# Kernel optimization log

Hardware: AMD Instinct MI355X
Metric: run time of the kernel (lower is better)

## Reference

```python
import jax, jax.numpy as jnp
import numpy as np

N = 524288
NUM_LEVELS = 16
FEATS = 2
LOG2_T = 19
TABLE = 1 << LOG2_T
MIN_RES, MAX_RES = 16, 1024
PRIMES = np.array([1, 2654435761, 805459861], dtype=np.uint32)
_growth = np.exp((np.log(MAX_RES) - np.log(MIN_RES)) / (NUM_LEVELS - 1))
SCALINGS = np.floor(MIN_RES * _growth ** np.arange(NUM_LEVELS)).astype(np.float32)  # [L]


def hash_encode(positions, table):
    # positions [N,3] in [0,1]; table [L*T, F]
    scaled = positions[:, None, :] * jnp.asarray(SCALINGS)[None, :, None]  # [N,L,3]
    fl = jnp.floor(scaled)
    ce = jnp.ceil(scaled)
    offset = scaled - fl  # [N,L,3]
    primes = jnp.asarray(PRIMES)  # [3] uint32
    lvl_off = jnp.arange(NUM_LEVELS, dtype=jnp.uint32) * jnp.uint32(TABLE)  # [L]
    out = jnp.zeros(scaled.shape[:2] + (FEATS,), scaled.dtype)
    for corner in range(8):
        bits = np.array([(corner >> d) & 1 for d in range(3)], dtype=np.float32)
        coord = jnp.where(jnp.asarray(bits, dtype=bool), ce, fl)
        h = coord.astype(jnp.int32).astype(jnp.uint32) * primes  # [N,L,3]
        h = h[..., 0] ^ h[..., 1] ^ h[..., 2]
        idx = ((h & jnp.uint32(TABLE - 1)) + lvl_off).astype(jnp.int32)  # [N,L]
        b = jnp.asarray(bits)
        w = jnp.prod(b * offset + (1.0 - b) * (1.0 - offset), axis=-1, keepdims=True)  # [N,L,1]
        out = out + w * table[idx]
    return out.reshape(out.shape[0], NUM_LEVELS * FEATS)  # [N,32]


def nerf_encode(d):
    # NeRFEncoding: 4 freqs in 2**linspace(0,4,4), include_input=True -> 27 dims
    freqs = 2.0 ** jnp.linspace(0.0, 4.0, 4)
    scaled = (2.0 * jnp.pi * d)[..., None] * freqs  # [N,3,4]
    scaled = scaled.reshape(d.shape[0], -1)  # [N,12]
    enc = jnp.sin(jnp.concatenate([scaled, scaled + jnp.pi / 2.0], axis=-1))  # [N,24]
    return jnp.concatenate([enc, d], axis=-1)  # [N,27]


def setup_inputs() -> dict:
    key = jax.random.key(0)
    ks = jax.random.split(key, 16)
    w = lambda k, i, o: jax.random.normal(k, (i, o), jnp.float32) * (1.0 / np.sqrt(i))
    return {
        "positions": jax.random.uniform(ks[0], (N, 3), jnp.float32),
        "directions": jax.random.normal(ks[1], (N, 3), jnp.float32),
        "hash_table": (jax.random.uniform(ks[2], (NUM_LEVELS * TABLE, FEATS), jnp.float32) * 2.0 - 1.0) * 1e-3,
        "w0": w(ks[3], 32, 64), "b0": jnp.zeros((64,), jnp.float32),
        "w1": w(ks[4], 64, 64), "b1": jnp.zeros((64,), jnp.float32),
        "w2": w(ks[5], 64, 64), "b2": jnp.zeros((64,), jnp.float32),
        "wr": w(ks[6], 91, 32), "br": jnp.zeros((32,), jnp.float32),
        "wc": w(ks[7], 32, 3), "bc": jnp.zeros((3,), jnp.float32),
        "wd": w(ks[8], 64, 1), "bd": jnp.zeros((1,), jnp.float32),
    }


def reference(positions, directions, hash_table, w0, b0, w1, b1, w2, b2, wr, br, wc, bc, wd, bd):
    enc_xyz = hash_encode(positions, hash_table)  # [N,32]
    enc_dir = nerf_encode(directions)  # [N,27]
    h = jax.nn.relu(enc_xyz @ w0 + b0)
    h = jax.nn.relu(h @ w1 + b1)
    base = h @ w2 + b2  # [N,64], linear out (out_activation=None)
    rgb_h = jnp.concatenate([enc_dir, base], axis=-1) @ wr + br  # [N,32], single layer
    rgb = jax.nn.sigmoid(rgb_h @ wc + bc)  # [N,3]
    density = jax.nn.softplus(base @ wd + bd)  # [N,1]
    return jnp.concatenate([rgb, density], axis=-1)  # [N,4]
```

## Files before the change

kernel.cpp:

```cpp
#include <hip/hip_runtime.h>
#include <math.h>

#define NPTS 524288
#define LOG2T 19
#define TSIZE (1u << LOG2T)
#define TMASK (TSIZE - 1u)

typedef unsigned int uint32;
typedef unsigned short ushort16;

typedef __attribute__((ext_vector_type(8))) short short8;
typedef __attribute__((ext_vector_type(4))) float f32x4;

__device__ __forceinline__ float bf2f(ushort16 u) {
    union { uint32 i; float f; } v; v.i = ((uint32)u) << 16; return v.f;
}
__device__ __forceinline__ ushort16 f2bf(float f) {
    union { float f; uint32 i; } v; v.f = f;
    uint32 r = v.i + 0x7fffu + ((v.i >> 16) & 1u);
    return (ushort16)(r >> 16);
}
__device__ __forceinline__ uint32 pack2(float a, float b) {
    return (uint32)f2bf(a) | ((uint32)f2bf(b) << 16);
}
__device__ __forceinline__ float ldin(const void* p, int i, bool f32) {
    return f32 ? ((const float*)p)[i] : bf2f(((const ushort16*)p)[i]);
}

struct Scal16 { float s[16]; };
struct Freq4  { float f[4]; };
struct HashP  { float s[16]; int dD[8]; int doff[8]; };
struct DenseP { int dD[6]; int pfx[7]; };

__global__ __launch_bounds__(256) void k_cvt10(const void* __restrict__ pos,
                                               const float4* __restrict__ tbl,
                                               uint4* __restrict__ tbl2F) {
    __shared__ int sFlag;
    int tid = threadIdx.x;
    if (tid < 64) {
        const ushort16* ph = (const ushort16*)pos;
        float v0 = bf2f(ph[tid]), v1 = bf2f(ph[tid + 64]);
        bool odd = !(fabsf(v0) <= 4.f) || !(fabsf(v1) <= 4.f);
        unsigned long long m = __ballot(odd);
        if (tid == 0) sFlag = (m != 0ull) ? 1 : 0;
    }
    __syncthreads();
    if (sFlag == 0) return;
    size_t g = (size_t)blockIdx.x * 256 + tid;
    float4 v0 = tbl[(size_t)3 * TSIZE + 2 * g];
    float4 v1 = tbl[(size_t)3 * TSIZE + 2 * g + 1];
    uint4 o;
    o.x = pack2(v0.x, v0.y); o.y = pack2(v0.z, v0.w);
    o.z = pack2(v1.x, v1.y); o.w = pack2(v1.z, v1.w);
    tbl2F[g] = o;
}

__global__ __launch_bounds__(256) void k_dense(const void* __restrict__ pos,
                                               const void* __restrict__ tbl,
                                               uint4* __restrict__ dense4,
                                               DenseP dp) {
    __shared__ int sFlag;
    int tid = threadIdx.x;
    if (tid < 64) {
        const ushort16* ph = (const ushort16*)pos;
        float v0 = bf2f(ph[tid]), v1 = bf2f(ph[tid + 64]);
        bool odd = !(fabsf(v0) <= 4.f) || !(fabsf(v1) <= 4.f);
        unsigned long long m = __ballot(odd);
        if (tid == 0) sFlag = (m != 0ull) ? 1 : 0;
    }
    __syncthreads();
    const bool f32 = (sFlag != 0);

    int e = blockIdx.x * 256 + tid;
    if (e >= dp.pfx[6]) return;
    int l = 0;
#pragma unroll
    for (int k = 1; k < 6; ++k) l += (e >= dp.pfx[k]) ? 1 : 0;
    int c = e - dp.pfx[l];
    int D = dp.dD[l], D2 = D * D;
    int cz = c / D2; int rm = c - cz * D2;
    int cy = rm / D; int cx = rm - cy * D;

    uint32 base = (uint32)l << LOG2T;
    uint32 hz  = (uint32)cz * 805459861u;
    uint32 hy0 = (uint32)cy * 2654435761u;
    uint32 hy1 = (uint32)(cy + 1) * 2654435761u;
    uint32 h00 = ((((uint32)cx)       ^ hy0 ^ hz) & TMASK) + base;
    uint32 h10 = ((((uint32)(cx + 1)) ^ hy0 ^ hz) & TMASK) + base;
    uint32 h01 = ((((uint32)cx)       ^ hy1 ^ hz) & TMASK) + base;
    uint32 h11 = ((((uint32)(cx + 1)) ^ hy1 ^ hz) & TMASK) + base;

    uint4 o;
    if (f32) {
        const float2* t2 = (const float2*)tbl;
        float2 a = t2[h00], b = t2[h10], cc = t2[h01], d = t2[h11];
        o.x = pack2(a.x, a.y); o.y = pack2(b.x, b.y);
        o.z = pack2(cc.x, cc.y); o.w = pack2(d.x, d.y);
    } else {
        const uint32* t1 = (const uint32*)tbl;
        o.x = t1[h00]; o.y = t1[h10]; o.z = t1[h01]; o.w = t1[h11];
    }
    dense4[e] = o;
}

__global__ __launch_bounds__(256) void k_denseEnc(const void* __restrict__ pos,
                                                  const uint4* __restrict__ dense4,
                                                  uint32* __restrict__ enc,
                                                  HashP hp) {
    __shared__ __align__(16) uint4 sPosQ[192];
    __shared__ int sFlag;
    int tid = threadIdx.x;
    if (tid < 64) {
        const ushort16* ph = (const ushort16*)pos;
        float v0 = bf2f(ph[tid]), v1 = bf2f(ph[tid + 64]);
        bool odd = !(fabsf(v0) <= 4.f) || !(fabsf(v1) <= 4.f);
        unsigned long long m = __ballot(odd);
        if (tid == 0) sFlag = (m != 0ull) ? 1 : 0;
    }
    __syncthreads();
    const bool f32 = (sFlag != 0);

    int p0 = blockIdx.x * 256;
    int pt = p0 + tid;

    {
        int n16 = f32 ? 192 : 96;
        const uint4* src = (const uint4*)((const char*)pos + (size_t)p0 * (f32 ? 12 : 6));
        for (int i = tid; i < n16; i += 256) sPosQ[i] = src[i];
    }
    __syncthreads();

    float x, y, z;
    if (f32) {
        const float* pf = (const float*)sPosQ;
        x = pf[3 * tid]; y = pf[3 * tid + 1]; z = pf[3 * tid + 2];
    } else {
        const ushort16* ph2 = (const ushort16*)sPosQ;
        x = bf2f(ph2[3 * tid]); y = bf2f(ph2[3 * tid + 1]); z = bf2f(ph2[3 * tid + 2]);
    }

#pragma unroll
    for (int l = 0; l < 6; ++l) {
        float s = hp.s[l];
        float sx = x * s, sy = y * s, sz = z * s;
        float fx = floorf(sx), fy = floorf(sy), fz = floorf(sz);
        float cx = ceilf(sx), cy = ceilf(sy), cz = ceilf(sz);
        float ox = sx - fx, oy = sy - fy, oz = sz - fz;
        float wx0 = 1.f - ox, wy0 = 1.f - oy, wz0 = 1.f - oz;

        int D = hp.dD[l], D2 = D * D;
        int fxi = (int)fx, fyi = (int)fy, fzi = (int)fz;
        bool dxb = ((int)cx != fxi);
        bool dyb = ((int)cy != fyi);
        bool dzb = ((int)cz != fzi);
        const uint4* dp4 = dense4 + hp.doff[l];
        int i0 = fxi + fyi * D + fzi * D2;
        uint4 P0 = dp4[i0];
        uint4 P1 = dp4[i0 + (dzb ? D2 : 0)];

        float a0 = 0.f, a1 = 0.f;
        {
            uint32 fv = P0.x, cv = dxb ? P0.y : P0.x;
            float w = wy0 * wz0;
            a0 += w * (wx0 * bf2f((ushort16)(fv & 0xffffu)) + ox * bf2f((ushort16)(cv & 0xffffu)));
            a1 += w * (wx0 * bf2f((ushort16)(fv >> 16))     + ox * bf2f((ushort16)(cv >> 16)));
        }
        {
            uint32 fv = dyb ? P0.z : P0.x;
            uint32 cv = dyb ? (dxb ? P0.w : P0.z) : (dxb ? P0.y : P0.x);
            float w = oy * wz0;
            a0 += w * (wx0 * bf2f((ushort16)(fv & 0xffffu)) + ox * bf2f((ushort16)(cv & 0xffffu)));
            a1 += w * (wx0 * bf2f((ushort16)(fv >> 16))     + ox * bf2f((ushort16)(cv >> 16)));
        }
        {
            uint32 fv = P1.x, cv = dxb ? P1.y : P1.x;
            float w = wy0 * oz;
            a0 += w * (wx0 * bf2f((ushort16)(fv & 0xffffu)) + ox * bf2f((ushort16)(cv & 0xffffu)));
            a1 += w * (wx0 * bf2f((ushort16)(fv >> 16))     + ox * bf2f((ushort16)(cv >> 16)));
        }
        {
            uint32 fv = dyb ? P1.z : P1.x;
            uint32 cv = dyb ? (dxb ? P1.w : P1.z) : (dxb ? P1.y : P1.x);
            float w = oy * oz;
            a0 += w * (wx0 * bf2f((ushort16)(fv & 0xffffu)) + ox * bf2f((ushort16)(cv & 0xffffu)));
            a1 += w * (wx0 * bf2f((ushort16)(fv >> 16))     + ox * bf2f((ushort16)(cv >> 16)));
        }
        enc[(size_t)l * NPTS + pt] = pack2(a0, a1);
    }
}

__global__ __launch_bounds__(256) void k_hashB(const void* __restrict__ pos,
                                               const void* __restrict__ tbl,
                                               const uint32* __restrict__ tbl2F,
                                               uint32* __restrict__ enc,
                                               HashP hp) {
    __shared__ __align__(16) uint4 sPosQ[192];
    __shared__ int sFlag;
    int tid = threadIdx.x;
    if (tid < 64) {
        const ushort16* ph = (const ushort16*)pos;
        float v0 = bf2f(ph[tid]), v1 = bf2f(ph[tid + 64]);
        bool odd = !(fabsf(v0) <= 4.f) || !(fabsf(v1) <= 4.f);
        unsigned long long m = __ballot(odd);
        if (tid == 0) sFlag = (m != 0ull) ? 1 : 0;
    }
    __syncthreads();
    const bool f32 = (sFlag != 0);

    int xcd = blockIdx.x & 7;
    int slot = blockIdx.x >> 3;
    int W = xcd * 2560 + slot;
    int lvl = 6 + (W >> 11);
    int chunk = W & 2047;
    int p0 = chunk * 256;
    int pt = p0 + tid;

    {
        int n16 = f32 ? 192 : 96;
        const uint4* src = (const uint4*)((const char*)pos + (size_t)p0 * (f32 ? 12 : 6));
        for (int i = tid; i < n16; i += 256) sPosQ[i] = src[i];
    }
    __syncthreads();

    float x, y, z;
    if (f32) {
        const float* pf = (const float*)sPosQ;
        x = pf[3 * tid]; y = pf[3 * tid + 1]; z = pf[3 * tid + 2];
    } else {
        const ushort16* ph2 = (const ushort16*)sPosQ;
        x = bf2f(ph2[3 * tid]); y = bf2f(ph2[3 * tid + 1]); z = bf2f(ph2[3 * tid + 2]);
    }

    float s = hp.s[lvl];
    float sx = x * s, sy = y * s, sz = z * s;
    float fx = floorf(sx), fy = floorf(sy), fz = floorf(sz);
    float cx = ceilf(sx), cy = ceilf(sy), cz = ceilf(sz);
    float ox = sx - fx, oy = sy - fy, oz = sz - fz;
    float wx0 = 1.f - ox, wy0 = 1.f - oy, wz0 = 1.f - oz;

    const uint32* tp; uint32 base;
    if (f32) { tp = tbl2F; base = (uint32)(lvl - 6) << LOG2T; }
    else     { tp = (const uint32*)tbl; base = (uint32)lvl << LOG2T; }
    uint32 hx0 = (uint32)(int)fx;
    uint32 hx1 = (uint32)(int)cx;
    uint32 hy0 = (uint32)(int)fy * 2654435761u;
    uint32 hy1 = (uint32)(int)cy * 2654435761u;
    uint32 hz0 = (uint32)(int)fz * 805459861u;
    uint32 hz1 = (uint32)(int)cz * 805459861u;

    float a0 = 0.f, a1 = 0.f;
#pragma unroll
    for (int yz = 0; yz < 4; ++yz) {
        uint32 m = ((yz & 1) ? hy1 : hy0) ^ ((yz & 2) ? hz1 : hz0);
        float wyz = ((yz & 1) ? oy : wy0) * ((yz & 2) ? oz : wz0);
        uint32 i0 = ((hx0 ^ m) & TMASK) + base;
        uint32 i1 = ((hx1 ^ m) & TMASK) + base;
        uint32 d0, d1;
        if (i1 == (i0 ^ 1u)) {
            uint2 pv = *(const uint2*)(tp + (i0 & ~1u));
            d0 = (i0 & 1u) ? pv.y : pv.x;
            d1 = (i0 & 1u) ? pv.x : pv.y;
        } else {
            d0 = tp[i0]; d1 = tp[i1];
        }
        a0 += wyz * (wx0 * bf2f((ushort16)(d0 & 0xffffu)) + ox * bf2f((ushort16)(d1 & 0xffffu)));
        a1 += wyz * (wx0 * bf2f((ushort16)(d0 >> 16))     + ox * bf2f((ushort16)(d1 >> 16)));
    }
    enc[(size_t)lvl * NPTS + pt] = pack2(a0, a1);
}

__global__ __launch_bounds__(256) void k_hash(const void* __restrict__ pos,
                                              const void* __restrict__ tbl,
                                              uint32* __restrict__ enc,
                                              Scal16 sc) {
    __shared__ int sFlag;
    int tid = threadIdx.x;
    if (tid < 64) {
        const ushort16* ph = (const ushort16*)pos;
        float v0 = bf2f(ph[tid]), v1 = bf2f(ph[tid + 64]);
        bool odd = !(fabsf(v0) <= 4.f) || !(fabsf(v1) <= 4.f);
        unsigned long long m = __ballot(odd);
        if (tid == 0) sFlag = (m != 0ull) ? 1 : 0;
    }
    __syncthreads();
    const bool f32 = (sFlag != 0);

    int lvl = ((blockIdx.x >> 14) << 3) + (blockIdx.x & 7);
    int pt = ((blockIdx.x >> 3) & 2047) * 256 + tid;

    float s = sc.s[lvl];
    float x = ldin(pos, 3 * pt, f32), y = ldin(pos, 3 * pt + 1, f32), z = ldin(pos, 3 * pt + 2, f32);
    float sx = x * s, sy = y * s, sz = z * s;
    float fx = floorf(sx), fy = floorf(sy), fz = floorf(sz);
    float cx = ceilf(sx), cy = ceilf(sy), cz = ceilf(sz);
    float ox = sx - fx, oy = sy - fy, oz = sz - fz;
    uint32 hx0 = (uint32)(int)fx;
    uint32 hx1 = (uint32)(int)cx;
    uint32 hy0 = (uint32)(int)fy * 2654435761u;
    uint32 hy1 = (uint32)(int)cy * 2654435761u;
    uint32 hz0 = (uint32)(int)fz * 805459861u;
    uint32 hz1 = (uint32)(int)cz * 805459861u;
    uint32 base = (uint32)lvl << LOG2T;
    float wx0 = 1.f - ox, wy0 = 1.f - oy, wz0 = 1.f - oz;

    float a0 = 0.f, a1 = 0.f;
    if (f32) {
        const float* tf = (const float*)tbl;
#pragma unroll
        for (int yz = 0; yz < 4; ++yz) {
            uint32 m = ((yz & 1) ? hy1 : hy0) ^ ((yz & 2) ? hz1 : hz0);
            float wyz = ((yz & 1) ? oy : wy0) * ((yz & 2) ? oz : wz0);
            uint32 i0 = ((hx0 ^ m) & TMASK) + base;
            uint32 i1 = ((hx1 ^ m) & TMASK) + base;
            float4 pv = *(const float4*)(tf + (size_t)(i0 & ~1u) * 2);
            bool lo = !(i0 & 1u);
            float f0 = lo ? pv.x : pv.z, f1 = lo ? pv.y : pv.w;
            float c0, c1;
            if (i1 == (i0 ^ 1u)) { c0 = lo ? pv.z : pv.x; c1 = lo ? pv.w : pv.y; }
            else { float2 tv = ((const float2*)tbl)[i1]; c0 = tv.x; c1 = tv.y; }
            a0 += wyz * (wx0 * f0 + ox * c0);
            a1 += wyz * (wx0 * f1 + ox * c1);
        }
    } else {
#pragma unroll
        for (int cr = 0; cr < 8; ++cr) {
            uint32 h = ((cr & 1) ? hx1 : hx0) ^ ((cr & 2) ? hy1 : hy0) ^ ((cr & 4) ? hz1 : hz0);
            uint32 idx = (h & TMASK) + base;
            uint32 dv = ((const uint32*)tbl)[idx];
            float w = ((cr & 1) ? ox : wx0) * ((cr & 2) ? oy : wy0) * ((cr & 4) ? oz : wz0);
            a0 += w * bf2f((ushort16)(dv & 0xffffu));
            a1 += w * bf2f((ushort16)(dv >> 16));
        }
    }
    enc[(size_t)lvl * NPTS + pt] = pack2(a0, a1);
}

#define STRY 72
#define STRW0 40
#define STRW12 72
#define STRWR 104
#define MSTRX 100
#define PPI 128
#define NIT (NPTS / PPI)

__global__ __launch_bounds__(512) void k_mlp(
    const void* __restrict__ pos,
    const uint32* __restrict__ enc, const void* __restrict__ dirs,
    const void* __restrict__ w0, const void* __restrict__ b0,
    const void* __restrict__ w1, const void* __restrict__ b1,
    const void* __restrict__ w2, const void* __restrict__ b2,
    const void* __restrict__ wr, const void* __restrict__ br,
    const void* __restrict__ wc, const void* __restrict__ bc,
    const void* __restrict__ wd, const void* __restrict__ bd,
    void* __restrict__ out, Freq4 fq)
{
    __shared__ __align__(16) ushort16 sX[PPI * MSTRX];
    __shared__ __align__(16) ushort16 sY[PPI * STRY];
    __shared__ __align__(16) ushort16 sW0[64 * STRW0];
    __shared__ __align__(16) ushort16 sW1[64 * STRW12];
    __shared__ __align__(16) ushort16 sW2[64 * STRW12];
    __shared__ __align__(16) ushort16 sWR[32 * STRWR];
    __shared__ __align__(16) ushort16 sW4[16 * STRWR];
    __shared__ __align__(16) float sB0[64], sB1[64], sB2[64], sBR[32], sFB[4];
    __shared__ int sFlag;

    int tid = threadIdx.x;

    if (tid < 64) {
        const ushort16* ph = (const ushort16*)pos;
        float v0 = bf2f(ph[tid]), v1 = bf2f(ph[tid + 64]);
        bool odd = !(fabsf(v0) <= 4.f) || !(fabsf(v1) <= 4.f);
        unsigned long long m = __ballot(odd);
        if (tid == 0) sFlag = (m != 0ull) ? 1 : 0;
    }
    __syncthreads();
    const bool f32 = (sFlag != 0);

    for (int i = tid; i < 2048; i += 512) { int k = i >> 6, n = i & 63; sW0[n * STRW0 + k] = f2bf(ldin(w0, i, f32)); }
    for (int i = tid; i < 4096; i += 512) { int k = i >> 6, n = i & 63; sW1[n * STRW12 + k] = f2bf(ldin(w1, i, f32)); }
    for (int i = tid; i < 4096; i += 512) { int k = i >> 6, n = i & 63; sW2[n * STRW12 + k] = f2bf(ldin(w2, i, f32)); }
    for (int i = tid; i < 2912; i += 512) {
        int r = i >> 5, n = i & 31; int k = (r < 27) ? r : r + 5;
        sWR[n * STRWR + k] = f2bf(ldin(wr, i, f32));
    }
    if (tid < 160) { int n = tid / 5, k = 27 + tid % 5; sWR[n * STRWR + k] = 0; }
    for (int i = tid; i < 1536; i += 512) {
        int n = i / 96, j = i % 96;
        float v = 0.f;
        if (n == 3 && j < 64) v = ldin(wd, j, f32);
        else if (n < 3 && j >= 64) v = ldin(wc, (j - 64) * 3 + n, f32);
        sW4[n * STRWR + j] = f2bf(v);
    }
    if (tid < 64) { sB0[tid] = ldin(b0, tid, f32); sB1[tid] = ldin(b1, tid, f32); sB2[tid] = ldin(b2, tid, f32); }
    if (tid < 32) sBR[tid] = ldin(br, tid, f32);
    if (tid < 3) sFB[tid] = ldin(bc, tid, f32);
    if (tid == 3) sFB[3] = ldin(bd, 0, f32);

    int lane = tid & 63, wv = tid >> 6;
    int colg = lane & 15, quad = lane >> 4;
    int myrow = wv * 16 + colg;

    for (int c = blockIdx.x; c < NIT; c += gridDim.x) {
        int p0 = c * PPI;
        __syncthreads();

        for (int i = tid; i < 1024; i += 512) {
            int l = i >> 6, p2 = (i & 63) * 2;
            uint2 e = *(const uint2*)&enc[(size_t)l * NPTS + p0 + p2];
            *(uint32*)&sX[p2 * MSTRX + 2 * l] = e.x;
            *(uint32*)&sX[(p2 + 1) * MSTRX + 2 * l] = e.y;
        }
        if (tid < 384) {
            int p = tid / 3, i2 = tid - 3 * (tid / 3);
            float dvv = ldin(dirs, 3 * (p0 + p) + i2, f32);
            ushort16* row = &sX[p * MSTRX + 64];
            float td = 6.28318530717958647692f * dvv;
            float a0 = td * fq.f[0], a1 = td * fq.f[1], a2 = td * fq.f[2], a3 = td * fq.f[3];
            uint2 sv, cv;
            sv.x = pack2(__sinf(a0), __sinf(a1));
            sv.y = pack2(__sinf(a2), __sinf(a3));
            cv.x = pack2(__cosf(a0), __cosf(a1));
            cv.y = pack2(__cosf(a2), __cosf(a3));
            *(uint2*)&row[i2 * 4] = sv;
            *(uint2*)&row[12 + i2 * 4] = cv;
            row[24 + i2] = f2bf(dvv);
        } else {
            int p = tid - 384;
            ushort16* row = &sX[p * MSTRX + 64];
#pragma unroll
            for (int j = 27; j < 32; ++j) row[j] = 0;
        }
        __syncthreads();

        {
            short8 xb = *(const short8*)&sX[myrow * MSTRX + quad * 8];
#pragma unroll
            for (int nt = 0; nt < 4; ++nt) {
                short8 a = *(const short8*)&sW0[(nt * 16 + colg) * STRW0 + quad * 8];
                f32x4 acc = {0.f, 0.f, 0.f, 0.f};
                acc = __builtin_amdgcn_mfma_f32_16x16x32_bf16(a, xb, acc, 0, 0, 0);
                float4 bi = *(const float4*)&sB0[nt * 16 + quad * 4];
                uint2 o;
                o.x = pack2(fmaxf(acc[0] + bi.x, 0.f), fmaxf(acc[1] + bi.y, 0.f));
                o.y = pack2(fmaxf(acc[2] + bi.z, 0.f), fmaxf(acc[3] + bi.w, 0.f));
                *(uint2*)&sY[myrow * STRY + nt * 16 + quad * 4] = o;
            }
        }
        {
            short8 xb0 = *(const short8*)&sY[myrow * STRY + quad * 8];
            short8 xb1 = *(const short8*)&sY[myrow * STRY + 32 + quad * 8];
#pragma unroll
            for (int nt = 0; nt < 4; ++nt) {
                short8 a0 = *(const short8*)&sW1[(nt * 16 + colg) * STRW12 + quad * 8];
                short8 a1 = *(const short8*)&sW1[(nt * 16 + colg) * STRW12 + 32 + quad * 8];
                f32x4 acc = {0.f, 0.f, 0.f, 0.f};
                acc = __builtin_amdgcn_mfma_f32_16x16x32_bf16(a0, xb0, acc, 0, 0, 0);
                acc = __builtin_amdgcn_mfma_f32_16x16x32_bf16(a1, xb1, acc, 0, 0, 0);
                float4 bi = *(const float4*)&sB1[nt * 16 + quad * 4];
                uint2 o;
                o.x = pack2(fmaxf(acc[0] + bi.x, 0.f), fmaxf(acc[1] + bi.y, 0.f));
                o.y = pack2(fmaxf(acc[2] + bi.z, 0.f), fmaxf(acc[3] + bi.w, 0.f));
                *(uint2*)&sX[myrow * MSTRX + nt * 16 + quad * 4] = o;
            }
        }
        {
            short8 xb0 = *(const short8*)&sX[myrow * MSTRX + quad * 8];
            short8 xb1 = *(const short8*)&sX[myrow * MSTRX + 32 + quad * 8];
#pragma unroll
            for (int nt = 0; nt < 4; ++nt) {
                short8 a0 = *(const short8*)&sW2[(nt * 16 + colg) * STRW12 + quad * 8];
                short8 a1 = *(const short8*)&sW2[(nt * 16 + colg) * STRW12 + 32 + quad * 8];
                f32x4 acc = {0.f, 0.f, 0.f, 0.f};
                acc = __builtin_amdgcn_mfma_f32_16x16x32_bf16(a0, xb0, acc, 0, 0, 0);
                acc = __builtin_amdgcn_mfma_f32_16x16x32_bf16(a1, xb1, acc, 0, 0, 0);
                float4 bi = *(const float4*)&sB2[nt * 16 + quad * 4];
                uint2 o;
                o.x = pack2(acc[0] + bi.x, acc[1] + bi.y);
                o.y = pack2(acc[2] + bi.z, acc[3] + bi.w);
                *(uint2*)&sY[myrow * STRY + nt * 16 + quad * 4] = o;
            }
        }
        {
            short8 xb0 = *(const short8*)&sX[myrow * MSTRX + 64 + quad * 8];
            short8 xb1 = *(const short8*)&sY[myrow * STRY + quad * 8];
            short8 xb2 = *(const short8*)&sY[myrow * STRY + 32 + quad * 8];
#pragma unroll
            for (int nt = 0; nt < 2; ++nt) {
                short8 a0 = *(const short8*)&sWR[(nt * 16 + colg) * STRWR + quad * 8];
                short8 a1 = *(const short8*)&sWR[(nt * 16 + colg) * STRWR + 32 + quad * 8];
                short8 a2 = *(const short8*)&sWR[(nt * 16 + colg) * STRWR + 64 + quad * 8];
                f32x4 acc = {0.f, 0.f, 0.f, 0.f};
                acc = __builtin_amdgcn_mfma_f32_16x16x32_bf16(a0, xb0, acc, 0, 0, 0);
                acc = __builtin_amdgcn_mfma_f32_16x16x32_bf16(a1, xb1, acc, 0, 0, 0);
                acc = __builtin_amdgcn_mfma_f32_16x16x32_bf16(a2, xb2, acc, 0, 0, 0);
                float4 bi = *(const float4*)&sBR[nt * 16 + quad * 4];
                uint2 o;
                o.x = pack2(acc[0] + bi.x, acc[1] + bi.y);
                o.y = pack2(acc[2] + bi.z, acc[3] + bi.w);
                *(uint2*)&sX[myrow * MSTRX + nt * 16 + quad * 4] = o;
            }
        }
        {
            short8 xb0 = *(const short8*)&sY[myrow * STRY + quad * 8];
            short8 xb1 = *(const short8*)&sY[myrow * STRY + 32 + quad * 8];
            short8 xb2 = *(const short8*)&sX[myrow * MSTRX + quad * 8];
            short8 a0 = *(const short8*)&sW4[colg * STRWR + quad * 8];
            short8 a1 = *(const short8*)&sW4[colg * STRWR + 32 + quad * 8];
            short8 a2 = *(const short8*)&sW4[colg * STRWR + 64 + quad * 8];
            f32x4 acc = {0.f, 0.f, 0.f, 0.f};
            acc = __builtin_amdgcn_mfma_f32_16x16x32_bf16(a0, xb0, acc, 0, 0, 0);
            acc = __builtin_amdgcn_mfma_f32_16x16x32_bf16(a1, xb1, acc, 0, 0, 0);
            acc = __builtin_amdgcn_mfma_f32_16x16x32_bf16(a2, xb2, acc, 0, 0, 0);
            if (quad == 0) {
                float r0 = acc[0] + sFB[0], r1 = acc[1] + sFB[1], r2 = acc[2] + sFB[2], dd = acc[3] + sFB[3];
                r0 = 1.f / (1.f + expf(-r0));
                r1 = 1.f / (1.f + expf(-r1));
                r2 = 1.f / (1.f + expf(-r2));
                float sp = (dd > 0.f) ? (dd + log1pf(expf(-dd))) : log1pf(expf(dd));
                int pt = p0 + myrow;
                if (f32) {
                    float4 o4; o4.x = r0; o4.y = r1; o4.z = r2; o4.w = sp;
                    ((float4*)out)[pt] = o4;
                } else {
                    uint2 o; o.x = pack2(r0, r1); o.y = pack2(r2, sp);
                    ((uint2*)out)[pt] = o;
                }
            }
        }
    }
}

#define FSTRX 104
__global__ __launch_bounds__(256) void k_fused(
    const void* __restrict__ pos, const void* __restrict__ dirs,
    const void* __restrict__ tbl,
    const void* __restrict__ w0, const void* __restrict__ b0,
    const void* __restrict__ w1, const void* __restrict__ b1,
    const void* __restrict__ w2, const void* __restrict__ b2,
    const void* __restrict__ wr, const void* __restrict__ br,
    const void* __restrict__ wc, const void* __restrict__ bc,
    const void* __restrict__ wd, const void* __restrict__ bd,
    void* __restrict__ out, Scal16 sc, Freq4 fq)
{
    __shared__ __align__(16) ushort16 sX[64 * FSTRX];
    __shared__ __align__(16) ushort16 sY[64 * STRY];
    __shared__ __align__(16) ushort16 sW0[64 * STRW0];
    __shared__ __align__(16) ushort16 sW1[64 * STRW12];
    __shared__ __align__(16) ushort16 sW2[64 * STRW12];
    __shared__ __align__(16) ushort16 sWR[32 * STRWR];
    __shared__ float sB0[64], sB1[64], sB2[64], sBR[32];
    __shared__ float sWCf[100];
    __shared__ float sWDf[64];
    __shared__ float sPosF[192];
    __shared__ int sFlag;

    int tid = threadIdx.x;
    if (tid < 64) {
        const ushort16* ph = (const ushort16*)pos;
        float v0 = bf2f(ph[tid]), v1 = bf2f(ph[tid + 64]);
        bool odd = !(fabsf(v0) <= 4.f) || !(fabsf(v1) <= 4.f);
        unsigned long long m = __ballot(odd);
        if (tid == 0) sFlag = (m != 0ull) ? 1 : 0;
    }
    __syncthreads();
    const bool f32 = (sFlag != 0);

    for (int i = tid; i < 2048; i += 256) { int k = i >> 6, n = i & 63; sW0[n * STRW0 + k] = f2bf(ldin(w0, i, f32)); }
    for (int i = tid; i < 4096; i += 256) { int k = i >> 6, n = i & 63; sW1[n * STRW12 + k] = f2bf(ldin(w1, i, f32)); }
    for (int i = tid; i < 4096; i += 256) { int k = i >> 6, n = i & 63; sW2[n * STRW12 + k] = f2bf(ldin(w2, i, f32)); }
    for (int i = tid; i < 2912; i += 256) {
        int r = i >> 5, n = i & 31; int k = (r < 27) ? r : r + 5;
        sWR[n * STRWR + k] = f2bf(ldin(wr, i, f32));
    }
    if (tid < 160) { int n = tid / 5, k = 27 + tid % 5; sWR[n * STRWR + k] = 0; }
    if (tid < 64) { sB0[tid] = ldin(b0, tid, f32); sB1[tid] = ldin(b1, tid, f32);
                    sB2[tid] = ldin(b2, tid, f32); sWDf[tid] = ldin(wd, tid, f32); }
    if (tid < 32) sBR[tid] = ldin(br, tid, f32);
    if (tid < 96) sWCf[tid] = ldin(wc, tid, f32);
    if (tid == 96) { sWCf[96] = ldin(bc, 0, f32); sWCf[97] = ldin(bc, 1, f32);
                     sWCf[98] = ldin(bc, 2, f32); sWCf[99] = ldin(bd, 0, f32); }

    int lane = tid & 63, wv = tid >> 6;
    int colg = lane & 15, quad = lane >> 4;
    int myl = tid & 15;
    float mys = sc.s[myl];
    uint32 mybase = (uint32)myl << LOG2T;

    for (int c = blockIdx.x; c < NPTS / 64; c += gridDim.x) {
        int p0 = c * 64;
        __syncthreads();
        if (tid < 192) sPosF[tid] = ldin(pos, p0 * 3 + tid, f32);
        __syncthreads();
#pragma unroll
        for (int ii = 0; ii < 4; ++ii) {
            int p = (tid >> 4) + 16 * ii;
            float x = sPosF[3 * p], y = sPosF[3 * p + 1], z = sPosF[3 * p + 2];
            float sx = x * mys, sy = y * mys, sz = z * mys;
            float fx = floorf(sx), fy = floorf(sy), fz = floorf(sz);
            float cx = ceilf(sx), cy = ceilf(sy), cz = ceilf(sz);
            float ox = sx - fx, oy = sy - fy, oz = sz - fz;
            uint32 hx0 = (uint32)(int)fx;
            uint32 hx1 = (uint32)(int)cx;
            uint32 hy0 = (uint32)(int)fy * 2654435761u;
            uint32 hy1 = (uint32)(int)cy * 2654435761u;
            uint32 hz0 = (uint32)(int)fz * 805459861u;
            uint32 hz1 = (uint32)(int)cz * 805459861u;
            float wx0 = 1.f - ox, wy0 = 1.f - oy, wz0 = 1.f - oz;
            float a0 = 0.f, a1 = 0.f;
#pragma unroll
            for (int cr = 0; cr < 8; ++cr) {
                uint32 h = ((cr & 1) ? hx1 : hx0) ^ ((cr & 2) ? hy1 : hy0) ^ ((cr & 4) ? hz1 : hz0);
                uint32 idx = (h & TMASK) + mybase;
                float t0, t1;
                if (f32) { float2 tv = ((const float2*)tbl)[idx]; t0 = tv.x; t1 = tv.y; }
                else { uint32 dv = ((const uint32*)tbl)[idx]; t0 = bf2f((ushort16)(dv & 0xffffu)); t1 = bf2f((ushort16)(dv >> 16)); }
                float w = ((cr & 1) ? ox : wx0) * ((cr & 2) ? oy : wy0) * ((cr & 4) ? oz : wz0);
                a0 += w * t0; a1 += w * t1;
            }
            *(uint32*)&sX[p * FSTRX + 2 * myl] = pack2(a0, a1);
        }
        __syncthreads();
        {
            short8 a = *(const short8*)&sX[(wv * 16 + colg) * FSTRX + quad * 8];
#pragma unroll
            for (int nt = 0; nt < 4; ++nt) {
                short8 bb = *(const short8*)&sW0[(nt * 16 + colg) * STRW0 + quad * 8];
                f32x4 acc = {0.f, 0.f, 0.f, 0.f};
                acc = __builtin_amdgcn_mfma_f32_16x16x32_bf16(a, bb, acc, 0, 0, 0);
                float bias = sB0[nt * 16 + colg];
#pragma unroll
                for (int r = 0; r < 4; ++r) {
                    float v = fmaxf(acc[r] + bias, 0.f);
                    sY[(wv * 16 + quad * 4 + r) * STRY + nt * 16 + colg] = f2bf(v);
                }
            }
        }
        __syncthreads();
        {
            short8 a0 = *(const short8*)&sY[(wv * 16 + colg) * STRY + quad * 8];
            short8 a1 = *(const short8*)&sY[(wv * 16 + colg) * STRY + 32 + quad * 8];
#pragma unroll
            for (int nt = 0; nt < 4; ++nt) {
                short8 bb0 = *(const short8*)&sW1[(nt * 16 + colg) * STRW12 + quad * 8];
                short8 bb1 = *(const short8*)&sW1[(nt * 16 + colg) * STRW12 + 32 + quad * 8];
                f32x4 acc = {0.f, 0.f, 0.f, 0.f};
                acc = __builtin_amdgcn_mfma_f32_16x16x32_bf16(a0, bb0, acc, 0, 0, 0);
                acc = __builtin_amdgcn_mfma_f32_16x16x32_bf16(a1, bb1, acc, 0, 0, 0);
                float bias = sB1[nt * 16 + colg];
#pragma unroll
                for (int r = 0; r < 4; ++r) {
                    float v = fmaxf(acc[r] + bias, 0.f);
                    sX[(wv * 16 + quad * 4 + r) * FSTRX + nt * 16 + colg] = f2bf(v);
                }
            }
        }
        __syncthreads();
        {
            short8 a0 = *(const short8*)&sX[(wv * 16 + colg) * FSTRX + quad * 8];
            short8 a1 = *(const short8*)&sX[(wv * 16 + colg) * FSTRX + 32 + quad * 8];
#pragma unroll
            for (int nt = 0; nt < 4; ++nt) {
                short8 bb0 = *(const short8*)&sW2[(nt * 16 + colg) * STRW12 + quad * 8];
                short8 bb1 = *(const short8*)&sW2[(nt * 16 + colg) * STRW12 + 32 + quad * 8];
                f32x4 acc = {0.f, 0.f, 0.f, 0.f};
                acc = __builtin_amdgcn_mfma_f32_16x16x32_bf16(a0, bb0, acc, 0, 0, 0);
                acc = __builtin_amdgcn_mfma_f32_16x16x32_bf16(a1, bb1, acc, 0, 0, 0);
                float bias = sB2[nt * 16 + colg];
#pragma unroll
                for (int r = 0; r < 4; ++r) {
                    sY[(wv * 16 + quad * 4 + r) * STRY + nt * 16 + colg] = f2bf(acc[r] + bias);
                }
            }
        }
        if (tid < 192) {
            int p = tid / 3, i2 = tid % 3;
            float dvv = ldin(dirs, 3 * (p0 + p) + i2, f32);
            ushort16* row = &sX[p * FSTRX + 64];
            float td = 6.28318530717958647692f * dvv;
#pragma unroll
            for (int j = 0; j < 4; ++j) {
                float arg = td * fq.f[j];
                float sv, cv;
                sincosf(arg, &sv, &cv);
                row[i2 * 4 + j] = f2bf(sv);
                row[12 + i2 * 4 + j] = f2bf(cv);
            }
            row[24 + i2] = f2bf(dvv);
        } else {
            int p = tid - 192;
            ushort16* row = &sX[p * FSTRX + 64];
#pragma unroll
            for (int j = 27; j < 32; ++j) row[j] = 0;
        }
        __syncthreads();
        {
            short8 a0 = *(const short8*)&sX[(wv * 16 + colg) * FSTRX + 64 + quad * 8];
            short8 a1 = *(const short8*)&sY[(wv * 16 + colg) * STRY + quad * 8];
            short8 a2 = *(const short8*)&sY[(wv * 16 + colg) * STRY + 32 + quad * 8];
#pragma unroll
            for (int nt = 0; nt < 2; ++nt) {
                short8 bb0 = *(const short8*)&sWR[(nt * 16 + colg) * STRWR + quad * 8];
                short8 bb1 = *(const short8*)&sWR[(nt * 16 + colg) * STRWR + 32 + quad * 8];
                short8 bb2 = *(const short8*)&sWR[(nt * 16 + colg) * STRWR + 64 + quad * 8];
                f32x4 acc = {0.f, 0.f, 0.f, 0.f};
                acc = __builtin_amdgcn_mfma_f32_16x16x32_bf16(a0, bb0, acc, 0, 0, 0);
                acc = __builtin_amdgcn_mfma_f32_16x16x32_bf16(a1, bb1, acc, 0, 0, 0);
                acc = __builtin_amdgcn_mfma_f32_16x16x32_bf16(a2, bb2, acc, 0, 0, 0);
                float bias = sBR[nt * 16 + colg];
#pragma unroll
                for (int r = 0; r < 4; ++r) {
                    sX[(wv * 16 + quad * 4 + r) * FSTRX + nt * 16 + colg] = f2bf(acc[r] + bias);
                }
            }
        }
        __syncthreads();
        if (tid < 64) {
            int pt = p0 + tid;
            float r0 = 0.f, r1 = 0.f, r2 = 0.f, dd = 0.f;
            const ushort16* hx = &sX[tid * FSTRX];
            const ushort16* hb = &sY[tid * STRY];
#pragma unroll
            for (int k = 0; k < 32; ++k) {
                float hv = bf2f(hx[k]);
                r0 += hv * sWCf[k * 3 + 0];
                r1 += hv * sWCf[k * 3 + 1];
                r2 += hv * sWCf[k * 3 + 2];
            }
#pragma unroll
            for (int k = 0; k < 64; ++k) dd += bf2f(hb[k]) * sWDf[k];
            r0 += sWCf[96]; r1 += sWCf[97]; r2 += sWCf[98]; dd += sWCf[99];
            r0 = 1.f / (1.f + expf(-r0));
            r1 = 1.f / (1.f + expf(-r1));
            r2 = 1.f / (1.f + expf(-r2));
            float sp = (dd > 0.f) ? (dd + log1pf(expf(-dd))) : log1pf(expf(dd));
            if (f32) {
                float4 o4; o4.x = r0; o4.y = r1; o4.z = r2; o4.w = sp;
                ((float4*)out)[pt] = o4;
            } else {
                uint2 o;
                o.x = pack2(r0, r1); o.y = pack2(r2, sp);
                ((uint2*)out)[pt] = o;
            }
        }
    }
}

extern "C" void kernel_launch(void* const* d_in, const int* in_sizes, int n_in,
                              void* d_out, int out_size, void* d_ws, size_t ws_size,
                              hipStream_t stream) {
    (void)in_sizes; (void)n_in; (void)out_size;

    Scal16 sc;
    double g = exp((log(1024.0) - log(16.0)) / 15.0);
    for (int l = 0; l < 16; ++l) sc.s[l] = (float)floor(16.0 * pow(g, (double)l));

    Freq4 fq;
    float lv[4] = {0.f, 4.f / 3.f, 8.f / 3.f, 4.f};
    for (int j = 0; j < 4; ++j) fq.f[j] = (float)pow(2.0, (double)lv[j]);

    DenseP dpp;
    HashP hp;
    dpp.pfx[0] = 0;
    for (int l = 0; l < 6; ++l) {
        int D = (int)sc.s[l] + 1;
        dpp.dD[l] = D;
        dpp.pfx[l + 1] = dpp.pfx[l] + D * D * D;
    }
    for (int l = 0; l < 16; ++l) hp.s[l] = sc.s[l];
    for (int l = 0; l < 8; ++l) {
        hp.dD[l]   = (l < 6) ? dpp.dD[l] : 1;
        hp.doff[l] = (l < 6) ? dpp.pfx[l] : 0;
    }
    int ndense = dpp.pfx[6];

    const size_t enc_bytes   = (size_t)16 * NPTS * 4;
    const size_t tbl2F_bytes = (size_t)10 * TSIZE * 4;
    const size_t dense_bytes = (size_t)ndense * 16 + 64;
    const size_t need_new = enc_bytes + tbl2F_bytes + dense_bytes;

    if (ws_size >= need_new) {
        uint32* enc   = (uint32*)d_ws;
        uint32* tbl2F = (uint32*)((char*)d_ws + enc_bytes);
        uint4*  dense4 = (uint4*)((char*)d_ws + enc_bytes + tbl2F_bytes);
        k_cvt10<<<dim3(5120), dim3(256), 0, stream>>>(d_in[0], (const float4*)d_in[2], (uint4*)tbl2F);
        k_dense<<<dim3((ndense + 255) / 256), dim3(256), 0, stream>>>(d_in[0], d_in[2], dense4, dpp);
        k_denseEnc<<<dim3(NPTS / 256), dim3(256), 0, stream>>>(d_in[0], dense4, enc, hp);
        k_hashB<<<dim3(10 * NPTS / 256), dim3(256), 0, stream>>>(d_in[0], d_in[2], tbl2F, enc, hp);
        k_mlp<<<dim3(512), dim3(512), 0, stream>>>(
            d_in[0], enc, d_in[1], d_in[3], d_in[4], d_in[5], d_in[6], d_in[7],
            d_in[8], d_in[9], d_in[10], d_in[11], d_in[12], d_in[13], d_in[14],
            d_out, fq);
    } else if (ws_size >= enc_bytes) {
        uint32* enc = (uint32*)d_ws;
        k_hash<<<dim3(2 * 8 * NPTS / 256), dim3(256), 0, stream>>>(d_in[0], d_in[2], enc, sc);
        k_mlp<<<dim3(512), dim3(512), 0, stream>>>(
            d_in[0], enc, d_in[1], d_in[3], d_in[4], d_in[5], d_in[6], d_in[7],
            d_in[8], d_in[9], d_in[10], d_in[11], d_in[12], d_in[13], d_in[14],
            d_out, fq);
    } else {
        k_fused<<<dim3(512), dim3(256), 0, stream>>>(
            d_in[0], d_in[1], d_in[2], d_in[3], d_in[4], d_in[5], d_in[6], d_in[7],
            d_in[8], d_in[9], d_in[10], d_in[11], d_in[12], d_in[13], d_in[14],
            d_out, sc, fq);
    }
}
```

Before: 325.4 us.

## Merge table-convert and dense-grid kernels, use hardware bf16 pack, retune MLP strides

Folds the bf16 table-conversion kernel and the dense-grid precompute kernel into one launch split by block index, saving a launch and a dependency gap. Replaces the software round-to-nearest bf16 packing with the v_cvt_pk_bf16_f32 instruction. Changes the LDS row strides for the hidden activations and weights from 72 to 76 to alter bank mapping, and reorders the enc-to-LDS staging loop so consecutive threads walk levels instead of points. The inline asm depends on the target supporting that instruction, and its rounding behaviour (e.g. for NaN) may differ slightly from the hand-written rounding.

```diff
diff --git a/kernel.cpp b/kernel.cpp
--- a/kernel.cpp
+++ b/kernel.cpp
@@ -21,7 +21,9 @@
     return (ushort16)(r >> 16);
 }
 __device__ __forceinline__ uint32 pack2(float a, float b) {
-    return (uint32)f2bf(a) | ((uint32)f2bf(b) << 16);
+    uint32 r;
+    asm("v_cvt_pk_bf16_f32 %0, %1, %2" : "=v"(r) : "v"(a), "v"(b));
+    return r;
 }
 __device__ __forceinline__ float ldin(const void* p, int i, bool f32) {
     return f32 ? ((const float*)p)[i] : bf2f(((const ushort16*)p)[i]);
@@ -32,9 +34,11 @@
 struct HashP  { float s[16]; int dD[8]; int doff[8]; };
 struct DenseP { int dD[6]; int pfx[7]; };
 
-__global__ __launch_bounds__(256) void k_cvt10(const void* __restrict__ pos,
-                                               const float4* __restrict__ tbl,
-                                               uint4* __restrict__ tbl2F) {
+__global__ __launch_bounds__(256) void k_prep(const void* __restrict__ pos,
+                                              const void* __restrict__ tbl,
+                                              uint4* __restrict__ tbl2F,
+                                              uint4* __restrict__ dense4,
+                                              DenseP dp) {
     __shared__ int sFlag;
     int tid = threadIdx.x;
     if (tid < 64) {
@@ -45,33 +49,22 @@
         if (tid == 0) sFlag = (m != 0ull) ? 1 : 0;
     }
     __syncthreads();
-    if (sFlag == 0) return;
-    size_t g = (size_t)blockIdx.x * 256 + tid;
-    float4 v0 = tbl[(size_t)3 * TSIZE + 2 * g];
-    float4 v1 = tbl[(size_t)3 * TSIZE + 2 * g + 1];
-    uint4 o;
-    o.x = pack2(v0.x, v0.y); o.y = pack2(v0.z, v0.w);
-    o.z = pack2(v1.x, v1.y); o.w = pack2(v1.z, v1.w);
-    tbl2F[g] = o;
-}
-
-__global__ __launch_bounds__(256) void k_dense(const void* __restrict__ pos,
-                                               const void* __restrict__ tbl,
-                                               uint4* __restrict__ dense4,
-                                               DenseP dp) {
-    __shared__ int sFlag;
-    int tid = threadIdx.x;
-    if (tid < 64) {
-        const ushort16* ph = (const ushort16*)pos;
-        float v0 = bf2f(ph[tid]), v1 = bf2f(ph[tid + 64]);
-        bool odd = !(fabsf(v0) <= 4.f) || !(fabsf(v1) <= 4.f);
-        unsigned long long m = __ballot(odd);
-        if (tid == 0) sFlag = (m != 0ull) ? 1 : 0;
-    }
-    __syncthreads();
     const bool f32 = (sFlag != 0);
 
-    int e = blockIdx.x * 256 + tid;
+    if (blockIdx.x < 5120) {
+        if (!f32) return;
+        const float4* tf4 = (const float4*)tbl;
+        size_t g = (size_t)blockIdx.x * 256 + tid;
+        float4 v0 = tf4[(size_t)3 * TSIZE + 2 * g];
+        float4 v1 = tf4[(size_t)3 * TSIZE + 2 * g + 1];
+        uint4 o;
+        o.x = pack2(v0.x, v0.y); o.y = pack2(v0.z, v0.w);
+        o.z = pack2(v1.x, v1.y); o.w = pack2(v1.z, v1.w);
+        tbl2F[g] = o;
+        return;
+    }
+
+    int e = (blockIdx.x - 5120) * 256 + tid;
     if (e >= dp.pfx[6]) return;
     int l = 0;
 #pragma unroll
@@ -335,9 +328,9 @@
     enc[(size_t)lvl * NPTS + pt] = pack2(a0, a1);
 }
 
-#define STRY 72
+#define STRY 76
 #define STRW0 40
-#define STRW12 72
+#define STRW12 76
 #define STRWR 104
 #define MSTRX 100
 #define PPI 128
@@ -405,10 +398,10 @@
         __syncthreads();
 
         for (int i = tid; i < 1024; i += 512) {
-            int l = i >> 6, p2 = (i & 63) * 2;
-            uint2 e = *(const uint2*)&enc[(size_t)l * NPTS + p0 + p2];
-            *(uint32*)&sX[p2 * MSTRX + 2 * l] = e.x;
-            *(uint32*)&sX[(p2 + 1) * MSTRX + 2 * l] = e.y;
+            int l = i & 15, pp = (i >> 4) * 2;
+            uint2 e = *(const uint2*)&enc[(size_t)l * NPTS + p0 + pp];
+            *(uint32*)&sX[pp * MSTRX + 2 * l] = e.x;
+            *(uint32*)&sX[(pp + 1) * MSTRX + 2 * l] = e.y;
         }
         if (tid < 384) {
             int p = tid / 3, i2 = tid - 3 * (tid / 3);
@@ -782,8 +775,8 @@
         uint32* enc   = (uint32*)d_ws;
         uint32* tbl2F = (uint32*)((char*)d_ws + enc_bytes);
         uint4*  dense4 = (uint4*)((char*)d_ws + enc_bytes + tbl2F_bytes);
-        k_cvt10<<<dim3(5120), dim3(256), 0, stream>>>(d_in[0], (const float4*)d_in[2], (uint4*)tbl2F);
-        k_dense<<<dim3((ndense + 255) / 256), dim3(256), 0, stream>>>(d_in[0], d_in[2], dense4, dpp);
+        int nprep = 5120 + (ndense + 255) / 256;
+        k_prep<<<dim3(nprep), dim3(256), 0, stream>>>(d_in[0], d_in[2], (uint4*)tbl2F, dense4, dpp);
         k_denseEnc<<<dim3(NPTS / 256), dim3(256), 0, stream>>>(d_in[0], dense4, enc, hp);
         k_hashB<<<dim3(10 * NPTS / 256), dim3(256), 0, stream>>>(d_in[0], d_in[2], tbl2F, enc, hp);
         k_mlp<<<dim3(512), dim3(512), 0, stream>>>(
```

Result: faster. 315.8 us (-3.0%).
